# Kernel tuning notes

Measured on AMD Instinct MI355X. Metric: run time of the kernel, lower is better.

The kernel has to match this reference:

```python
import jax, jax.numpy as jnp
import numpy as np
import math

N = 50000          # n_nodes
E = 1600000        # n_edges (avg degree 32)
D = 256            # input_size
H = 8              # n_heads
HS = D // H        # head_size = 32


def setup_inputs() -> dict:
    key = jax.random.key(0)
    k1, k2, k3, k4, k5 = jax.random.split(key, 5)
    X = jax.random.normal(k1, (N, D), dtype=jnp.float32)
    # xavier_uniform for [D, HS] weight: bound = sqrt(6 / (fan_in + fan_out))
    bound = math.sqrt(6.0 / (D + HS))
    Wq = jax.random.uniform(k2, (D, HS), jnp.float32, -bound, bound)
    Wk = jax.random.uniform(k3, (D, HS), jnp.float32, -bound, bound)
    Wv = jax.random.uniform(k4, (D, HS), jnp.float32, -bound, bound)
    edge_index = jax.random.randint(k5, (2, E), 0, N, dtype=jnp.int32)
    return {"X": X, "Wq": Wq, "Wk": Wk, "Wv": Wv, "edge_index": edge_index}


def reference(X, Wq, Wk, Wv, edge_index):
    # Projections: [N, HS]
    Q = X @ Wq
    K = X @ Wk
    V = X @ Wv
    r = edge_index[0]  # row (query) node per edge
    c = edge_index[1]  # col (key/value) node per edge
    dk = jnp.asarray(math.sqrt(HS), dtype=X.dtype)
    # Edge-level attention logits: [E]
    scores = jnp.sum(Q[r] * K[c], axis=-1) / dk
    # Sparse row-wise (dim=1) softmax over existing edges only.
    row_max = jax.ops.segment_max(scores, r, num_segments=N)   # -inf for empty rows
    ex = jnp.exp(scores - row_max[r])                          # [E]
    denom = jax.ops.segment_sum(ex, r, num_segments=N)         # [N]
    # Weighted V aggregation: [N, HS]
    num = jax.ops.segment_sum(ex[:, None] * V[c], r, num_segments=N)
    # Rows with no incident edges produce zeros (matches sparse softmax + to_dense @ V).
    safe = jnp.maximum(denom, jnp.asarray(1e-30, X.dtype))[:, None]
    return jnp.where(denom[:, None] > 0, num / safe, jnp.zeros_like(num))
```

## Files before the change

kernel.cpp:

```cpp
#include <hip/hip_runtime.h>

#define N_NODES 50000
#define N_EDGES 1600000
#define D_IN    256
#define HS      32

#define NB      400
#define ROWS_PB 125
#define CAP     5120
#define EPB     4096

#define MTILE   64
#define XPITCH  264

typedef __bf16 bf16x8 __attribute__((ext_vector_type(8)));
typedef float  floatx4 __attribute__((ext_vector_type(4)));

static __device__ __forceinline__ unsigned short f2bf(float f) {
    unsigned u = __float_as_uint(f);
    return (unsigned short)((u + 0x7FFFu + ((u >> 16) & 1u)) >> 16);
}

__global__ __launch_bounds__(256) void wfrag_kernel(
    const float* __restrict__ Wq, const float* __restrict__ Wk,
    const float* __restrict__ Wv, unsigned short* __restrict__ wfrag,
    int* __restrict__ fill, int* __restrict__ rowptr)
{
    if (blockIdx.x == 0) {
        for (int b = threadIdx.x; b < NB; b += 256) fill[b] = 0;
        if (threadIdx.x == 0) rowptr[N_NODES] = N_EDGES;
    }
    const int i = blockIdx.x * blockDim.x + threadIdx.x;
    if (i >= 8 * 6 * 64 * 8) return;
    const int j    = i & 7;
    const int lane = (i >> 3) & 63;
    const int st   = i >> 9;
    const int t    = st % 6;
    const int s    = st / 6;
    const int k    = s * 32 + (lane >> 4) * 8 + j;
    const int col  = t * 16 + (lane & 15);
    float v;
    if      (col < 32) v = Wq[k * HS + col];
    else if (col < 64) v = Wk[k * HS + (col - 32)];
    else               v = Wv[k * HS + (col - 64)];
    wfrag[i] = f2bf(v);
}

__global__ __launch_bounds__(256) void proj_mfma_kernel(
    const float* __restrict__ X, const unsigned short* __restrict__ wfrag,
    float* __restrict__ Q, unsigned int* __restrict__ KVp)
{
    __shared__ unsigned short xs[MTILE * XPITCH];

    const int t    = threadIdx.x;
    const int lane = t & 63;
    const int w    = t >> 6;
    const int quad = lane >> 4;
    const int m16  = lane & 15;
    const int row0 = blockIdx.x * MTILE;

#pragma unroll
    for (int it = 0; it < (MTILE * 64) / 256; it++) {
        const int idx = it * 256 + t;
        const int r   = idx >> 6;
        const int c4  = idx & 63;
        int gr = row0 + r;
        if (gr >= N_NODES) gr = N_NODES - 1;
        const float4 xv = *(const float4*)(X + (size_t)gr * D_IN + c4 * 4);
        ushort4 b;
        b.x = f2bf(xv.x); b.y = f2bf(xv.y); b.z = f2bf(xv.z); b.w = f2bf(xv.w);
        *(ushort4*)(&xs[r * XPITCH + c4 * 4]) = b;
    }
    __syncthreads();

    floatx4 acc[6];
#pragma unroll
    for (int nt = 0; nt < 6; nt++) acc[nt] = (floatx4)0.f;

    const int arow = w * 16 + m16;

#pragma unroll
    for (int s = 0; s < 8; s++) {
        bf16x8 bfr[6];
#pragma unroll
        for (int nt = 0; nt < 6; nt++)
            bfr[nt] = *(const bf16x8*)(wfrag + (((s * 6 + nt) * 64 + lane) * 8));
        const bf16x8 afr = *(const bf16x8*)(&xs[arow * XPITCH + s * 32 + quad * 8]);
#pragma unroll
        for (int nt = 0; nt < 6; nt++)
            acc[nt] = __builtin_amdgcn_mfma_f32_16x16x32_bf16(afr, bfr[nt], acc[nt], 0, 0, 0);
    }

#pragma unroll
    for (int i = 0; i < 4; i++) {
        const int gr = row0 + w * 16 + quad * 4 + i;
        if (gr < N_NODES) {
#pragma unroll
            for (int nt = 0; nt < 2; nt++)
                Q[gr * HS + nt * 16 + m16] = acc[nt][i];
#pragma unroll
            for (int p = 0; p < 2; p++) {
                const int j = p * 16 + m16;
                const unsigned kb = f2bf(acc[2 + p][i]);
                const unsigned vb = f2bf(acc[4 + p][i]);
                KVp[gr * HS + j] = (kb << 16) | vb;
            }
        }
    }
}

__global__ __launch_bounds__(256) void bin_kernel(
    const int* __restrict__ er, const int* __restrict__ ec,
    int* __restrict__ fill, unsigned int* __restrict__ pairs)
{
    __shared__ int lcnt[NB];
    const int t  = threadIdx.x;
    const int e0 = blockIdx.x * EPB;
    const int e1 = min(e0 + EPB, N_EDGES);

    for (int b = t; b < NB; b += 256) lcnt[b] = 0;
    __syncthreads();

    int rl[16], cl[16];
#pragma unroll
    for (int i = 0; i < 16; i++) {
        const int e = e0 + t + i * 256;
        if (e < e1) {
            rl[i] = er[e];
            cl[i] = ec[e];
            atomicAdd(&lcnt[rl[i] / ROWS_PB], 1);
        }
    }
    __syncthreads();

    for (int b = t; b < NB; b += 256) {
        const int c = lcnt[b];
        lcnt[b] = (c > 0) ? atomicAdd(&fill[b], c) : 0;
    }
    __syncthreads();

#pragma unroll
    for (int i = 0; i < 16; i++) {
        const int e = e0 + t + i * 256;
        if (e < e1) {
            const int r = rl[i];
            const int b = r / ROWS_PB;
            const int slot = atomicAdd(&lcnt[b], 1);
            pairs[(size_t)b * CAP + slot] =
                ((unsigned)(r - b * ROWS_PB) << 16) | (unsigned)cl[i];
        }
    }
}

__global__ __launch_bounds__(512) void scanfill_kernel(
    const int* __restrict__ fill, int* __restrict__ bstart)
{
    __shared__ int s[512];
    const int t = threadIdx.x;
    const int v = (t < NB) ? fill[t] : 0;
    s[t] = v;
    __syncthreads();
#pragma unroll
    for (int ofs = 1; ofs < 512; ofs <<= 1) {
        const int u = (t >= ofs) ? s[t - ofs] : 0;
        __syncthreads();
        s[t] += u;
        __syncthreads();
    }
    if (t < NB) bstart[t] = s[t] - v;
}

__global__ __launch_bounds__(256) void place_kernel(
    const unsigned int* __restrict__ pairs, const int* __restrict__ fill,
    const int* __restrict__ bstart, int* __restrict__ rowptr,
    int* __restrict__ col_sorted)
{
    __shared__ int cnt_l[ROWS_PB];
    __shared__ int s[128];
    __shared__ int stage[CAP];

    const int b = blockIdx.x;
    const int t = threadIdx.x;
    const int n = fill[b];
    const int base = bstart[b];
    const unsigned int* pb = pairs + (size_t)b * CAP;

    for (int i = t; i < ROWS_PB; i += 256) cnt_l[i] = 0;
    __syncthreads();

    unsigned pl[20];
#pragma unroll
    for (int k = 0; k < 20; k++) {
        const int i = t + k * 256;
        if (i < n) {
            pl[k] = pb[i];
            atomicAdd(&cnt_l[pl[k] >> 16], 1);
        }
    }
    __syncthreads();

    if (t < 128) s[t] = (t < ROWS_PB) ? cnt_l[t] : 0;
    __syncthreads();
#pragma unroll
    for (int ofs = 1; ofs < 128; ofs <<= 1) {
        const int u = (t < 128 && t >= ofs) ? s[t - ofs] : 0;
        __syncthreads();
        if (t < 128) s[t] += u;
        __syncthreads();
    }
    int excl = 0;
    if (t < ROWS_PB) {
        excl = s[t] - cnt_l[t];
        rowptr[b * ROWS_PB + t] = base + excl;
    }
    __syncthreads();
    if (t < ROWS_PB) cnt_l[t] = excl;
    __syncthreads();

#pragma unroll
    for (int k = 0; k < 20; k++) {
        const int i = t + k * 256;
        if (i < n) {
            const unsigned p = pl[k];
            const int pos = atomicAdd(&cnt_l[p >> 16], 1);
            stage[pos] = (int)(p & 0xFFFFu);
        }
    }
    __syncthreads();

    for (int i = t; i < n; i += 256)
        col_sorted[base + i] = stage[i];
}

__global__ __launch_bounds__(256) void aggregate_kernel(
    const int* __restrict__ rowptr, const int* __restrict__ col,
    const float* __restrict__ Q, const unsigned int* __restrict__ KVp,
    float* __restrict__ out)
{
    const int lane = threadIdx.x & 63;
    const int r    = (blockIdx.x * blockDim.x + threadIdx.x) >> 6;
    if (r >= N_NODES) return;
    const int comp = lane & 7;
    const int slot = lane >> 3;

    const float4 q4 = *(const float4*)(Q + r * HS + comp * 4);
    const int start = rowptr[r];
    const int end   = rowptr[r + 1];
    const int last  = end - 1;
    const float scale = 0.17677669529663687f;

    float accD = 0.f;
    float n0 = 0.f, n1 = 0.f, n2 = 0.f, n3 = 0.f;

    for (int e0 = start; e0 < end; e0 += 32) {
        int   cc[4];
        uint4 kv[4];
#pragma unroll
        for (int b = 0; b < 4; b++)
            if (e0 + 8 * b < end)
                cc[b] = col[min(e0 + 8 * b + slot, last)];
#pragma unroll
        for (int b = 0; b < 4; b++)
            if (e0 + 8 * b < end)
                kv[b] = *(const uint4*)(KVp + (size_t)cc[b] * HS + comp * 4);
#pragma unroll
        for (int b = 0; b < 4; b++) {
            if (e0 + 8 * b < end) {
                float p = q4.x * __uint_as_float(kv[b].x & 0xFFFF0000u)
                        + q4.y * __uint_as_float(kv[b].y & 0xFFFF0000u)
                        + q4.z * __uint_as_float(kv[b].z & 0xFFFF0000u)
                        + q4.w * __uint_as_float(kv[b].w & 0xFFFF0000u);
#pragma unroll
                for (int ofs = 1; ofs < 8; ofs <<= 1)
                    p += __shfl_xor(p, ofs, 64);
                const float ex = (e0 + 8 * b + slot < end) ? __expf(p * scale) : 0.f;
                accD += ex;
                n0 += ex * __uint_as_float(kv[b].x << 16);
                n1 += ex * __uint_as_float(kv[b].y << 16);
                n2 += ex * __uint_as_float(kv[b].z << 16);
                n3 += ex * __uint_as_float(kv[b].w << 16);
            }
        }
    }

#pragma unroll
    for (int ofs = 8; ofs < 64; ofs <<= 1) {
        accD += __shfl_xor(accD, ofs, 64);
        n0 += __shfl_xor(n0, ofs, 64);
        n1 += __shfl_xor(n1, ofs, 64);
        n2 += __shfl_xor(n2, ofs, 64);
        n3 += __shfl_xor(n3, ofs, 64);
    }

    if (slot == 0) {
        const float inv = (accD > 0.f) ? 1.f / accD : 0.f;
        float4 o;
        o.x = n0 * inv; o.y = n1 * inv; o.z = n2 * inv; o.w = n3 * inv;
        *(float4*)(out + r * HS + comp * 4) = o;
    }
}

extern "C" void kernel_launch(void* const* d_in, const int* in_sizes, int n_in,
                              void* d_out, int out_size, void* d_ws, size_t ws_size,
                              hipStream_t stream)
{
    const float* X  = (const float*)d_in[0];
    const float* Wq = (const float*)d_in[1];
    const float* Wk = (const float*)d_in[2];
    const float* Wv = (const float*)d_in[3];
    const int*   ei = (const int*)d_in[4];
    const int* er = ei;
    const int* ec = ei + N_EDGES;

    float* out = (float*)d_out;

    float* Q          = (float*)d_ws;
    unsigned int* KVp = (unsigned int*)(Q + (size_t)N_NODES * HS);
    int* fill         = (int*)(KVp + (size_t)N_NODES * HS);
    int* bstart       = fill + NB;
    int* rowptr       = bstart + NB;
    unsigned short* wfrag = (unsigned short*)(rowptr + (N_NODES + 1));
    unsigned int* pairs   = (unsigned int*)(wfrag + 8 * 6 * 64 * 8);
    int* col_sorted   = (int*)(pairs + (size_t)NB * CAP);

    wfrag_kernel<<<(8 * 6 * 64 * 8 + 255) / 256, 256, 0, stream>>>(
        Wq, Wk, Wv, wfrag, fill, rowptr);
    proj_mfma_kernel<<<(N_NODES + MTILE - 1) / MTILE, 256, 0, stream>>>(X, wfrag, Q, KVp);

    bin_kernel<<<(N_EDGES + EPB - 1) / EPB, 256, 0, stream>>>(er, ec, fill, pairs);
    scanfill_kernel<<<1, 512, 0, stream>>>(fill, bstart);
    place_kernel<<<NB, 256, 0, stream>>>(pairs, fill, bstart, rowptr, col_sorted);

    aggregate_kernel<<<(N_NODES * 64 + 255) / 256, 256, 0, stream>>>(
        rowptr, col_sorted, Q, KVp, out);
}
```

Before: 165.5 us.

## Fuse projection and edge binning into one launch; fold prefix scan into placement

Projection and edge-binning now run as one grid, interleaved in a 2:1 pattern: two projection tiles for each binning block, with the binning counters reusing the projection's shared-memory buffer. The separate single-block scan kernel is removed. Each place block instead sums the fill counts of all earlier buckets with a block reduction to get its base offset. This removes two kernel launches and lets the independent projection and binning work overlap on the GPU. In exchange, every place block re-reads up to 400 fill counts and does a reduction, which is redundant work.

```diff
diff --git a/kernel.cpp b/kernel.cpp
--- a/kernel.cpp
+++ b/kernel.cpp
@@ -12,6 +12,8 @@
 
 #define MTILE   64
 #define XPITCH  264
+#define PROJ_B  ((N_NODES + MTILE - 1) / MTILE)
+#define BIN_B   ((N_EDGES + EPB - 1) / EPB)
 
 typedef __bf16 bf16x8 __attribute__((ext_vector_type(8)));
 typedef float  floatx4 __attribute__((ext_vector_type(4)));
@@ -46,147 +48,139 @@
     wfrag[i] = f2bf(v);
 }
 
-__global__ __launch_bounds__(256) void proj_mfma_kernel(
+__global__ __launch_bounds__(256) void proj_bin_kernel(
     const float* __restrict__ X, const unsigned short* __restrict__ wfrag,
-    float* __restrict__ Q, unsigned int* __restrict__ KVp)
-{
-    __shared__ unsigned short xs[MTILE * XPITCH];
-
-    const int t    = threadIdx.x;
-    const int lane = t & 63;
-    const int w    = t >> 6;
-    const int quad = lane >> 4;
-    const int m16  = lane & 15;
-    const int row0 = blockIdx.x * MTILE;
-
-#pragma unroll
-    for (int it = 0; it < (MTILE * 64) / 256; it++) {
-        const int idx = it * 256 + t;
-        const int r   = idx >> 6;
-        const int c4  = idx & 63;
-        int gr = row0 + r;
-        if (gr >= N_NODES) gr = N_NODES - 1;
-        const float4 xv = *(const float4*)(X + (size_t)gr * D_IN + c4 * 4);
-        ushort4 b;
-        b.x = f2bf(xv.x); b.y = f2bf(xv.y); b.z = f2bf(xv.z); b.w = f2bf(xv.w);
-        *(ushort4*)(&xs[r * XPITCH + c4 * 4]) = b;
-    }
-    __syncthreads();
-
-    floatx4 acc[6];
-#pragma unroll
-    for (int nt = 0; nt < 6; nt++) acc[nt] = (floatx4)0.f;
-
-    const int arow = w * 16 + m16;
-
-#pragma unroll
-    for (int s = 0; s < 8; s++) {
-        bf16x8 bfr[6];
-#pragma unroll
-        for (int nt = 0; nt < 6; nt++)
-            bfr[nt] = *(const bf16x8*)(wfrag + (((s * 6 + nt) * 64 + lane) * 8));
-        const bf16x8 afr = *(const bf16x8*)(&xs[arow * XPITCH + s * 32 + quad * 8]);
-#pragma unroll
-        for (int nt = 0; nt < 6; nt++)
-            acc[nt] = __builtin_amdgcn_mfma_f32_16x16x32_bf16(afr, bfr[nt], acc[nt], 0, 0, 0);
-    }
-
-#pragma unroll
-    for (int i = 0; i < 4; i++) {
-        const int gr = row0 + w * 16 + quad * 4 + i;
-        if (gr < N_NODES) {
-#pragma unroll
-            for (int nt = 0; nt < 2; nt++)
-                Q[gr * HS + nt * 16 + m16] = acc[nt][i];
-#pragma unroll
-            for (int p = 0; p < 2; p++) {
-                const int j = p * 16 + m16;
-                const unsigned kb = f2bf(acc[2 + p][i]);
-                const unsigned vb = f2bf(acc[4 + p][i]);
-                KVp[gr * HS + j] = (kb << 16) | vb;
-            }
-        }
-    }
-}
-
-__global__ __launch_bounds__(256) void bin_kernel(
+    float* __restrict__ Q, unsigned int* __restrict__ KVp,
     const int* __restrict__ er, const int* __restrict__ ec,
     int* __restrict__ fill, unsigned int* __restrict__ pairs)
 {
-    __shared__ int lcnt[NB];
-    const int t  = threadIdx.x;
-    const int e0 = blockIdx.x * EPB;
-    const int e1 = min(e0 + EPB, N_EDGES);
-
-    for (int b = t; b < NB; b += 256) lcnt[b] = 0;
-    __syncthreads();
-
-    int rl[16], cl[16];
-#pragma unroll
-    for (int i = 0; i < 16; i++) {
-        const int e = e0 + t + i * 256;
-        if (e < e1) {
-            rl[i] = er[e];
-            cl[i] = ec[e];
-            atomicAdd(&lcnt[rl[i] / ROWS_PB], 1);
-        }
-    }
-    __syncthreads();
-
-    for (int b = t; b < NB; b += 256) {
-        const int c = lcnt[b];
-        lcnt[b] = (c > 0) ? atomicAdd(&fill[b], c) : 0;
-    }
-    __syncthreads();
-
-#pragma unroll
-    for (int i = 0; i < 16; i++) {
-        const int e = e0 + t + i * 256;
-        if (e < e1) {
-            const int r = rl[i];
-            const int b = r / ROWS_PB;
-            const int slot = atomicAdd(&lcnt[b], 1);
-            pairs[(size_t)b * CAP + slot] =
-                ((unsigned)(r - b * ROWS_PB) << 16) | (unsigned)cl[i];
-        }
-    }
-}
-
-__global__ __launch_bounds__(512) void scanfill_kernel(
-    const int* __restrict__ fill, int* __restrict__ bstart)
-{
-    __shared__ int s[512];
+    __shared__ __align__(16) unsigned short xs[MTILE * XPITCH];
+
     const int t = threadIdx.x;
-    const int v = (t < NB) ? fill[t] : 0;
-    s[t] = v;
-    __syncthreads();
-#pragma unroll
-    for (int ofs = 1; ofs < 512; ofs <<= 1) {
-        const int u = (t >= ofs) ? s[t - ofs] : 0;
-        __syncthreads();
-        s[t] += u;
-        __syncthreads();
-    }
-    if (t < NB) bstart[t] = s[t] - v;
+    const int mod = blockIdx.x % 3;
+
+    if (mod != 2) {
+        const int pb   = (blockIdx.x / 3) * 2 + mod;
+        const int lane = t & 63;
+        const int w    = t >> 6;
+        const int quad = lane >> 4;
+        const int m16  = lane & 15;
+        const int row0 = pb * MTILE;
+
+#pragma unroll
+        for (int it = 0; it < (MTILE * 64) / 256; it++) {
+            const int idx = it * 256 + t;
+            const int r   = idx >> 6;
+            const int c4  = idx & 63;
+            int gr = row0 + r;
+            if (gr >= N_NODES) gr = N_NODES - 1;
+            const float4 xv = *(const float4*)(X + (size_t)gr * D_IN + c4 * 4);
+            ushort4 b;
+            b.x = f2bf(xv.x); b.y = f2bf(xv.y); b.z = f2bf(xv.z); b.w = f2bf(xv.w);
+            *(ushort4*)(&xs[r * XPITCH + c4 * 4]) = b;
+        }
+        __syncthreads();
+
+        floatx4 acc[6];
+#pragma unroll
+        for (int nt = 0; nt < 6; nt++) acc[nt] = (floatx4)0.f;
+
+        const int arow = w * 16 + m16;
+
+#pragma unroll
+        for (int s = 0; s < 8; s++) {
+            bf16x8 bfr[6];
+#pragma unroll
+            for (int nt = 0; nt < 6; nt++)
+                bfr[nt] = *(const bf16x8*)(wfrag + (((s * 6 + nt) * 64 + lane) * 8));
+            const bf16x8 afr = *(const bf16x8*)(&xs[arow * XPITCH + s * 32 + quad * 8]);
+#pragma unroll
+            for (int nt = 0; nt < 6; nt++)
+                acc[nt] = __builtin_amdgcn_mfma_f32_16x16x32_bf16(afr, bfr[nt], acc[nt], 0, 0, 0);
+        }
+
+#pragma unroll
+        for (int i = 0; i < 4; i++) {
+            const int gr = row0 + w * 16 + quad * 4 + i;
+            if (gr < N_NODES) {
+#pragma unroll
+                for (int nt = 0; nt < 2; nt++)
+                    Q[gr * HS + nt * 16 + m16] = acc[nt][i];
+#pragma unroll
+                for (int p = 0; p < 2; p++) {
+                    const int j = p * 16 + m16;
+                    const unsigned kb = f2bf(acc[2 + p][i]);
+                    const unsigned vb = f2bf(acc[4 + p][i]);
+                    KVp[gr * HS + j] = (kb << 16) | vb;
+                }
+            }
+        }
+    } else {
+        int* lcnt = (int*)xs;
+        const int bb = blockIdx.x / 3;
+        const int e0 = bb * EPB;
+        const int e1 = min(e0 + EPB, N_EDGES);
+
+        for (int b = t; b < NB; b += 256) lcnt[b] = 0;
+        __syncthreads();
+
+        int rl[16], cl[16];
+#pragma unroll
+        for (int i = 0; i < 16; i++) {
+            const int e = e0 + t + i * 256;
+            if (e < e1) {
+                rl[i] = er[e];
+                cl[i] = ec[e];
+                atomicAdd(&lcnt[rl[i] / ROWS_PB], 1);
+            }
+        }
+        __syncthreads();
+
+        for (int b = t; b < NB; b += 256) {
+            const int c = lcnt[b];
+            lcnt[b] = (c > 0) ? atomicAdd(&fill[b], c) : 0;
+        }
+        __syncthreads();
+
+#pragma unroll
+        for (int i = 0; i < 16; i++) {
+            const int e = e0 + t + i * 256;
+            if (e < e1) {
+                const int r = rl[i];
+                const int b = r / ROWS_PB;
+                const int slot = atomicAdd(&lcnt[b], 1);
+                pairs[(size_t)b * CAP + slot] =
+                    ((unsigned)(r - b * ROWS_PB) << 16) | (unsigned)cl[i];
+            }
+        }
+    }
 }
 
 __global__ __launch_bounds__(256) void place_kernel(
     const unsigned int* __restrict__ pairs, const int* __restrict__ fill,
-    const int* __restrict__ bstart, int* __restrict__ rowptr,
-    int* __restrict__ col_sorted)
+    int* __restrict__ rowptr, int* __restrict__ col_sorted)
 {
     __shared__ int cnt_l[ROWS_PB];
     __shared__ int s[128];
+    __shared__ int red[256];
     __shared__ int stage[CAP];
 
     const int b = blockIdx.x;
     const int t = threadIdx.x;
     const int n = fill[b];
-    const int base = bstart[b];
     const unsigned int* pb = pairs + (size_t)b * CAP;
 
+    int partial = 0;
+    for (int i = t; i < b; i += 256) partial += fill[i];
+    red[t] = partial;
     for (int i = t; i < ROWS_PB; i += 256) cnt_l[i] = 0;
     __syncthreads();
+#pragma unroll
+    for (int ofs = 128; ofs > 0; ofs >>= 1) {
+        if (t < ofs) red[t] += red[t + ofs];
+        __syncthreads();
+    }
+    const int base = red[0];
 
     unsigned pl[20];
 #pragma unroll
@@ -317,19 +311,18 @@
     float* Q          = (float*)d_ws;
     unsigned int* KVp = (unsigned int*)(Q + (size_t)N_NODES * HS);
     int* fill         = (int*)(KVp + (size_t)N_NODES * HS);
-    int* bstart       = fill + NB;
-    int* rowptr       = bstart + NB;
+    int* rowptr       = fill + NB;
     unsigned short* wfrag = (unsigned short*)(rowptr + (N_NODES + 1));
     unsigned int* pairs   = (unsigned int*)(wfrag + 8 * 6 * 64 * 8);
     int* col_sorted   = (int*)(pairs + (size_t)NB * CAP);
 
     wfrag_kernel<<<(8 * 6 * 64 * 8 + 255) / 256, 256, 0, stream>>>(
         Wq, Wk, Wv, wfrag, fill, rowptr);
-    proj_mfma_kernel<<<(N_NODES + MTILE - 1) / MTILE, 256, 0, stream>>>(X, wfrag, Q, KVp);
-
-    bin_kernel<<<(N_EDGES + EPB - 1) / EPB, 256, 0, stream>>>(er, ec, fill, pairs);
-    scanfill_kernel<<<1, 512, 0, stream>>>(fill, bstart);
-    place_kernel<<<NB, 256, 0, stream>>>(pairs, fill, bstart, rowptr, col_sorted);
+
+    proj_bin_kernel<<<PROJ_B + BIN_B, 256, 0, stream>>>(
+        X, wfrag, Q, KVp, er, ec, fill, pairs);
+
+    place_kernel<<<NB, 256, 0, stream>>>(pairs, fill, rowptr, col_sorted);
 
     aggregate_kernel<<<(N_NODES * 64 + 255) / 256, 256, 0, stream>>>(
         rowptr, col_sorted, Q, KVp, out);
```

New measurement: 158.9 us, median of 2. 4.0% less time.
